# Performance work log

Hardware: AMD Instinct MI355X
Metric: run time of the kernel (lower is better)

## Reference

```python
import jax, jax.numpy as jnp
import numpy as np

FRAME_LEN = 400
HOP = 160
FFT_LEN = 512
PREEMPH = 0.97
MEL_FLOOR = 1.192092955078125e-07


def _hertz_to_mel(freq):
    return 1127.0 * np.log(1.0 + freq / 700.0)


def _mel_filter_bank(num_frequency_bins=256, num_mel_filters=80, min_frequency=20.0,
                     max_frequency=8000.0, sampling_rate=16000):
    mel_min = _hertz_to_mel(min_frequency)
    mel_max = _hertz_to_mel(max_frequency)
    mel_freqs = np.linspace(mel_min, mel_max, num_mel_filters + 2)
    # NOTE: source has filter_freqs = mel_freqs (mel-space, intentional replication of bug)
    filter_freqs = mel_freqs
    fft_bin_width = sampling_rate / (num_frequency_bins * 2)
    fft_freqs = _hertz_to_mel(fft_bin_width * np.arange(num_frequency_bins))
    filter_diff = np.diff(filter_freqs)
    slopes = filter_freqs[None, :] - fft_freqs[:, None]          # [256, 82]
    down_slopes = -slopes[:, :-2] / filter_diff[:-1]
    up_slopes = slopes[:, 2:] / filter_diff[1:]
    fb = np.maximum(0.0, np.minimum(down_slopes, up_slopes))      # [256, 80]
    # F.pad(mel_filters, (0,0,0,1)) -> one extra zero row -> [257, 80]
    return np.pad(fb, ((0, 1), (0, 0))).astype(np.float32)


def _window():
    n = np.arange(FRAME_LEN)
    hann = 0.5 - 0.5 * np.cos(2.0 * np.pi * n / (FRAME_LEN - 1))  # periodic=False
    return (hann ** 0.85).astype(np.float32)


def setup_inputs() -> dict:
    key = jax.random.key(0)
    T = 9_600_000  # 10 min @ 16 kHz
    raw_speech = jax.random.normal(key, (1, T), dtype=jnp.float32)
    return {
        "raw_speech": raw_speech,
        "mel_filters": jnp.asarray(_mel_filter_bank()),  # [257, 80]
        "window": jnp.asarray(_window()),                # [400]
    }


def reference(raw_speech, mel_filters, window):
    wav = raw_speech.reshape(-1) * 32768.0  # * 2**15
    num_frames = 1 + (wav.shape[0] - FRAME_LEN) // HOP
    idx = jnp.arange(num_frames)[:, None] * HOP + jnp.arange(FRAME_LEN)[None, :]
    frames = wav[idx]                                         # [F, 400]
    frames = frames - frames.mean(axis=1, keepdims=True)      # remove DC offset
    # preemphasis: y[0] = x[0]*(1-p), y[n] = x[n] - p*x[n-1]
    pre = jnp.concatenate(
        [frames[:, :1] * (1.0 - PREEMPH), frames[:, 1:] - PREEMPH * frames[:, :-1]],
        axis=1,
    )
    pre = pre * window
    padded = jnp.pad(pre, ((0, 0), (0, FFT_LEN - FRAME_LEN)))  # [F, 512]
    spec = jnp.abs(jnp.fft.rfft(padded, axis=1)) ** 2          # [F, 257]
    mel = jnp.log(jnp.maximum(spec @ mel_filters, MEL_FLOOR))  # [F, 80]
    mean = mel.mean(axis=0, keepdims=True)
    var = mel.var(axis=0, keepdims=True, ddof=1)               # unbiased
    return (mel - mean) / jnp.sqrt(var + 1e-7)
```

## Files before the change

### kernel.cpp

```cpp
#include <hip/hip_runtime.h>
#include <math.h>

#define FRAME_LEN 400
#define HOP 160
#define NMEL 80
#define PREEMPH 0.97f
#define MEL_FLOOR 1.192092955078125e-07f
#define WAVES 4
#define PPW 4
#define PPB (WAVES*PPW)

__device__ __forceinline__ float2 cadd(float2 a, float2 b){ return make_float2(a.x+b.x, a.y+b.y); }
__device__ __forceinline__ float2 csub(float2 a, float2 b){ return make_float2(a.x-b.x, a.y-b.y); }
__device__ __forceinline__ float2 cmul(float2 a, float2 b){ return make_float2(a.x*b.x-a.y*b.y, a.x*b.y+a.y*b.x); }

__device__ __forceinline__ float bperm(int addr, float v) {
    return __int_as_float(__builtin_amdgcn_ds_bpermute(addr, __float_as_int(v)));
}
template<int C>
__device__ __forceinline__ float dppf(float v) {
    return __int_as_float(__builtin_amdgcn_update_dpp(0, __float_as_int(v), C, 0xF, 0xF, false));
}
__device__ __forceinline__ float wscan_add(float v) {
    v += __int_as_float(__builtin_amdgcn_update_dpp(0, __float_as_int(v), 0x111, 0xF, 0xF, false));
    v += __int_as_float(__builtin_amdgcn_update_dpp(0, __float_as_int(v), 0x112, 0xF, 0xF, false));
    v += __int_as_float(__builtin_amdgcn_update_dpp(0, __float_as_int(v), 0x114, 0xF, 0xF, false));
    v += __int_as_float(__builtin_amdgcn_update_dpp(0, __float_as_int(v), 0x118, 0xF, 0xF, false));
    v += __int_as_float(__builtin_amdgcn_update_dpp(0, __float_as_int(v), 0x142, 0xA, 0xF, false));
    v += __int_as_float(__builtin_amdgcn_update_dpp(0, __float_as_int(v), 0x143, 0xC, 0xF, false));
    return v;
}

__global__ __launch_bounds__(256) void feat_kernel(
    const float* __restrict__ raw, const float* __restrict__ window,
    float* __restrict__ mel_out, double* __restrict__ accum, int F)
{
    __shared__ __align__(16) float wlds[FRAME_LEN];
    __shared__ __align__(16) float xu[WAVES][560];
    __shared__ __align__(16) float pfx[WAVES][2][256];

    float* uu = xu[0];
    int*   ks = (int*)xu[1];

    const int t = threadIdx.x;
    const int l = t & 63;
    const int w = t >> 6;

    if (t < FRAME_LEN) wlds[t] = window[t] * 32768.f;
    if (t + 256 < FRAME_LEN) wlds[t + 256] = window[t + 256] * 32768.f;
    const double mel_min = 1127.0 * log(1.0 + 20.0 / 700.0);
    const double mel_max = 1127.0 * log(1.0 + 8000.0 / 700.0);
    const double dstep = (mel_max - mel_min) / 81.0;
    {
        double fhz = 31.25 * (double)t;
        double m = 1127.0 * log(1.0 + fhz / 700.0);
        uu[t] = (float)((m - mel_min) / dstep);
    }
    __syncthreads();
    if (t < 82) {
        double fhz = 700.0 * (exp((mel_min + (double)t * dstep) / 1127.0) - 1.0);
        int k = (int)ceil(fhz / 31.25);
        k = max(0, min(256, k));
        while (k > 0 && uu[k - 1] >= (float)t) --k;
        while (k < 256 && uu[k] < (float)t) ++k;
        ks[t] = k;
    }

    const int bl   = __brev((unsigned)l) >> 26;
    const int adrX = (l ^ 63) << 2;
    const int adr0 = ((64 - l) & 63) << 2;

    float2 dt[5];
    float  sg[6];
    #pragma unroll
    for (int j = 0; j < 6; ++j) {
        int d = 1 << j;
        sg[j] = (l & d) ? -1.f : 1.f;
        if (j >= 1) {
            float2 tw = make_float2(1.f, 0.f);
            if (l & d) {
                float tt = (float)(l & (d - 1));
                float ang = -3.1415926535897932f * tt / (float)d;
                sincosf(ang, &tw.y, &tw.x);
            }
            dt[j - 1] = tw;
        }
    }
    float2 w2[4];
    #pragma unroll
    for (int q = 1; q < 4; ++q) {
        float ang = -6.283185307179586f * (float)(bl * q) * (1.0f / 256.0f);
        sincosf(ang, &w2[q].y, &w2[q].x);
    }
    float2 wk[4];
    #pragma unroll
    for (int q = 0; q < 4; ++q) {
        int k = 4 * l + q;
        float ang = -3.1415926535897932f * (float)k * (1.0f / 256.0f);
        sincosf(ang, &wk[q].y, &wk[q].x);
    }
    __syncthreads();

    float fr1[4];
    #pragma unroll
    for (int q = 0; q < 4; ++q) {
        float u = uu[4 * l + q];
        fr1[q] = u - floorf(u);
    }
    int a0 = ks[l], b0 = ks[l + 1], e0 = ks[l + 2];
    int a1 = 1, b1 = 1, e1 = 1;
    if (l < 16) { a1 = ks[64 + l]; b1 = ks[65 + l]; e1 = ks[66 + l]; }
    __syncthreads();

    float* xw = xu[w];
    const int NP = (F + 1) >> 1;
    const int basePair = blockIdx.x * PPB + w * PPW;

    float acc_s0 = 0.f, acc_q0 = 0.f;
    float acc_s1 = 0.f, acc_q1 = 0.f;

    for (int fi = 0; fi < PPW; ++fi) {
        int P = basePair + fi;
        if (P >= NP) break;
        int fA = 2 * P;
        bool hasB = (fA + 1) < F;

        const float4* g4 = (const float4*)(raw + (size_t)fA * HOP);
        float4 a = g4[l];
        float4 b = make_float4(0.f, 0.f, 0.f, 0.f);
        float4 c = make_float4(0.f, 0.f, 0.f, 0.f);
        if (hasB || l < 36) b = g4[64 + l];
        if (hasB && l < 12) c = g4[128 + l];
        float as = a.x + a.y + a.z + a.w;
        float bs = b.x + b.y + b.z + b.w;
        float cs = c.x + c.y + c.z + c.w;
        float sA8 = as + (l < 36 ? bs : 0.f);
        float sB8 = (l >= 40 ? as : 0.f) + bs + cs;
        float totA = __int_as_float(__builtin_amdgcn_readlane(__float_as_int(wscan_add(sA8)), 63));
        float totB = __int_as_float(__builtin_amdgcn_readlane(__float_as_int(wscan_add(sB8)), 63));
        float KA = totA * (1.0f / (float)FRAME_LEN) * (1.0f - PREEMPH);
        float KB = totB * (1.0f / (float)FRAME_LEN) * (1.0f - PREEMPH);

        ((float4*)xw)[l] = a;
        ((float4*)xw)[64 + l] = b;
        if (l < 12) ((float4*)xw)[128 + l] = c;

        float2 Z[2][4];
        #pragma unroll
        for (int r = 0; r < 4; ++r) {
            int off = 128 * r + 2 * bl;
            if (off < FRAME_LEN) {
                float2 xA = *(const float2*)(xw + off);
                float2 xB = *(const float2*)(xw + 160 + off);
                float xm1A = (off == 0) ? xA.x : xw[off - 1];
                float xm1B = (off == 0) ? xB.x : xw[159 + off];
                float2 wn  = *(const float2*)(wlds + off);
                Z[0][r] = make_float2((fmaf(-PREEMPH, xm1A, xA.x) - KA) * wn.x,
                                      (fmaf(-PREEMPH, xA.x,  xA.y) - KA) * wn.y);
                Z[1][r] = make_float2((fmaf(-PREEMPH, xm1B, xB.x) - KB) * wn.x,
                                      (fmaf(-PREEMPH, xB.x,  xB.y) - KB) * wn.y);
            } else {
                Z[0][r] = make_float2(0.f, 0.f);
                Z[1][r] = make_float2(0.f, 0.f);
            }
        }

        #pragma unroll
        for (int s = 0; s < 2; ++s) {
            float2 t0 = cadd(Z[s][0], Z[s][2]);
            float2 t1 = csub(Z[s][0], Z[s][2]);
            float2 t2 = cadd(Z[s][1], Z[s][3]);
            float2 t3 = csub(Z[s][1], Z[s][3]);
            Z[s][0] = cadd(t0, t2);
            Z[s][2] = csub(t0, t2);
            Z[s][1] = make_float2(t1.x + t3.y, t1.y - t3.x);
            Z[s][3] = make_float2(t1.x - t3.y, t1.y + t3.x);
            #pragma unroll
            for (int q = 1; q < 4; ++q) Z[s][q] = cmul(Z[s][q], w2[q]);
        }

        #pragma unroll
        for (int s = 0; s < 2; ++s)
        #pragma unroll
        for (int q = 0; q < 4; ++q) {
            float ox = dppf<0xB1>(Z[s][q].x), oy = dppf<0xB1>(Z[s][q].y);
            Z[s][q].x = fmaf(sg[0], Z[s][q].x, ox);
            Z[s][q].y = fmaf(sg[0], Z[s][q].y, oy);
        }
        #pragma unroll
        for (int s = 0; s < 2; ++s)
        #pragma unroll
        for (int q = 0; q < 4; ++q) {
            float2 Zw = cmul(Z[s][q], dt[0]);
            float ox = dppf<0x4E>(Zw.x), oy = dppf<0x4E>(Zw.y);
            Z[s][q].x = fmaf(sg[1], Zw.x, ox);
            Z[s][q].y = fmaf(sg[1], Zw.y, oy);
        }
        #pragma unroll
        for (int s = 0; s < 2; ++s)
        #pragma unroll
        for (int q = 0; q < 4; ++q) {
            float2 Zw = cmul(Z[s][q], dt[1]);
            float ox = __shfl_xor(Zw.x, 4, 64), oy = __shfl_xor(Zw.y, 4, 64);
            Z[s][q].x = fmaf(sg[2], Zw.x, ox);
            Z[s][q].y = fmaf(sg[2], Zw.y, oy);
        }
        #pragma unroll
        for (int s = 0; s < 2; ++s)
        #pragma unroll
        for (int q = 0; q < 4; ++q) {
            float2 Zw = cmul(Z[s][q], dt[2]);
            float ox = dppf<0x128>(Zw.x), oy = dppf<0x128>(Zw.y);
            Z[s][q].x = fmaf(sg[3], Zw.x, ox);
            Z[s][q].y = fmaf(sg[3], Zw.y, oy);
        }
        #pragma unroll
        for (int s = 0; s < 2; ++s)
        #pragma unroll
        for (int q = 0; q < 4; ++q) {
            float2 Zw = cmul(Z[s][q], dt[3]);
            float ox = __shfl_xor(Zw.x, 16, 64), oy = __shfl_xor(Zw.y, 16, 64);
            Z[s][q].x = fmaf(sg[4], Zw.x, ox);
            Z[s][q].y = fmaf(sg[4], Zw.y, oy);
        }
        #pragma unroll
        for (int s = 0; s < 2; ++s)
        #pragma unroll
        for (int q = 0; q < 4; ++q) {
            float2 Zw = cmul(Z[s][q], dt[4]);
            float ox = __shfl_xor(Zw.x, 32, 64), oy = __shfl_xor(Zw.y, 32, 64);
            Z[s][q].x = fmaf(sg[5], Zw.x, ox);
            Z[s][q].y = fmaf(sg[5], Zw.y, oy);
        }

        #pragma unroll
        for (int s = 0; s < 2; ++s) {
            float zcr[4], zci[4];
            zcr[0] = bperm(adr0, Z[s][0].x);
            zci[0] = bperm(adr0, Z[s][0].y);
            zcr[1] = bperm(adrX, Z[s][3].x);
            zci[1] = bperm(adrX, Z[s][3].y);
            zcr[2] = bperm(adrX, Z[s][2].x);
            zci[2] = bperm(adrX, Z[s][2].y);
            zcr[3] = bperm(adrX, Z[s][1].x);
            zci[3] = bperm(adrX, Z[s][1].y);

            float pw[4], pv[4];
            #pragma unroll
            for (int q = 0; q < 4; ++q) {
                float Er = 0.5f * (Z[s][q].x + zcr[q]);
                float Ei = 0.5f * (Z[s][q].y - zci[q]);
                float Or = 0.5f * (Z[s][q].y + zci[q]);
                float Oi = 0.5f * (zcr[q] - Z[s][q].x);
                float Xr = Er + Or * wk[q].x - Oi * wk[q].y;
                float Xi = Ei + Or * wk[q].y + Oi * wk[q].x;
                pw[q] = Xr * Xr + Xi * Xi;
                pv[q] = pw[q] * fr1[q];
            }
            float A0 = pw[0], A1 = A0 + pw[1], A2 = A1 + pw[2], A3 = A2 + pw[3];
            float B0 = pv[0], B1 = B0 + pv[1], B2 = B1 + pv[2], B3 = B2 + pv[3];
            float sA = wscan_add(A3);
            float sB = wscan_add(B3);
            float exA = sA - A3;
            float exB = sB - B3;
            float* pP = pfx[w][0];
            float* pF = pfx[w][1];
            ((float4*)pP)[l] = make_float4(exA + A0, exA + A1, exA + A2, exA + A3);
            ((float4*)pF)[l] = make_float4(exB + B0, exB + B1, exB + B2, exB + B3);

            int f = fA + s;
            bool act = (s == 0) || hasB;
            if (act) {
                float E1a = pF[a0 - 1], E1b = pF[b0 - 1], E1e = pF[e0 - 1];
                float EAb = pP[b0 - 1], EAe = pP[e0 - 1];
                float acc = fmaf(2.f, E1b, -E1a) - E1e + (EAe - EAb);
                float v = __logf(fmaxf(acc, MEL_FLOOR));
                mel_out[(size_t)f * NMEL + l] = v;
                acc_s0 += v; acc_q0 = fmaf(v, v, acc_q0);
                if (l < 16) {
                    float F1a = pF[a1 - 1], F1b = pF[b1 - 1], F1e = pF[e1 - 1];
                    float FAb = pP[b1 - 1], FAe = pP[e1 - 1];
                    float ac2 = fmaf(2.f, F1b, -F1a) - F1e + (FAe - FAb);
                    float v1 = __logf(fmaxf(ac2, MEL_FLOOR));
                    mel_out[(size_t)f * NMEL + 64 + l] = v1;
                    acc_s1 += v1; acc_q1 = fmaf(v1, v1, acc_q1);
                }
            }
        }
    }

    {
        float* red = pfx[w][0];
        red[l] = acc_s0;
        red[80 + l] = acc_q0;
        if (l < 16) { red[64 + l] = acc_s1; red[144 + l] = acc_q1; }
    }
    __syncthreads();
    if (t < 160) {
        float tot = pfx[0][0][t] + pfx[1][0][t] + pfx[2][0][t] + pfx[3][0][t];
        atomicAdd(&accum[t], (double)tot);
    }
}

__global__ __launch_bounds__(256) void norm_kernel(
    float* __restrict__ mel, const double* __restrict__ accum, int F)
{
    __shared__ float s_mean[NMEL], s_inv[NMEL];
    int t = threadIdx.x;
    if (t < NMEL) {
        double S = accum[t], Q = accum[NMEL + t];
        double mean = S / (double)F;
        double var = (Q - S * S / (double)F) / (double)(F - 1);
        s_mean[t] = (float)mean;
        s_inv[t]  = (float)(1.0 / sqrt(var + 1e-7));
    }
    __syncthreads();
    unsigned n = (unsigned)F * NMEL;
    unsigned stride = gridDim.x * 256u * 4u;
    unsigned i = (blockIdx.x * 256u + (unsigned)t) * 4u;
    int c = (int)(i % NMEL);
    float m0 = s_mean[c],     r0 = s_inv[c];
    float m1 = s_mean[c + 1], r1 = s_inv[c + 1];
    float m2 = s_mean[c + 2], r2 = s_inv[c + 2];
    float m3 = s_mean[c + 3], r3 = s_inv[c + 3];
    for (; i < n; i += stride) {
        float4 v = *(float4*)(mel + i);
        v.x = (v.x - m0) * r0;
        v.y = (v.y - m1) * r1;
        v.z = (v.z - m2) * r2;
        v.w = (v.w - m3) * r3;
        *(float4*)(mel + i) = v;
    }
}

extern "C" void kernel_launch(void* const* d_in, const int* in_sizes, int n_in,
                              void* d_out, int out_size, void* d_ws, size_t ws_size,
                              hipStream_t stream)
{
    const float* raw = (const float*)d_in[0];
    const float* window = (const float*)d_in[2];
    float* out = (float*)d_out;

    int N = in_sizes[0];
    int F = 1 + (N - FRAME_LEN) / HOP;
    double* accum = (double*)d_ws;

    hipMemsetAsync(d_ws, 0, 2 * NMEL * sizeof(double), stream);
    int NP = (F + 1) / 2;
    int gridA = (NP + PPB - 1) / PPB;
    feat_kernel<<<gridA, 256, 0, stream>>>(raw, window, out, accum, F);
    norm_kernel<<<2560, 256, 0, stream>>>(out, accum, F);
}
```

Baseline: 153.8 us.

## Process four overlapping frames per wave iteration instead of two

Each wave now loads a 880-sample window covering four consecutive frames (hop 160) and runs the FFT, power and mel stages on four frames at once, where it previously handled two. This raises reuse of the loaded samples, since four frames need 880 samples instead of 2x560, and gives more independent work per iteration to hide latency. In exchange, register pressure roughly doubles (Z[4][4] complex values), and LDS grows, with prefix buffers double-buffered by frame parity. The tail uses bounds-checked loads against N/4.

```diff
diff --git a/kernel.cpp b/kernel.cpp
--- a/kernel.cpp
+++ b/kernel.cpp
@@ -7,8 +7,8 @@
 #define PREEMPH 0.97f
 #define MEL_FLOOR 1.192092955078125e-07f
 #define WAVES 4
-#define PPW 4
-#define PPB (WAVES*PPW)
+#define QPW 2
+#define QPB (WAVES*QPW)
 
 __device__ __forceinline__ float2 cadd(float2 a, float2 b){ return make_float2(a.x+b.x, a.y+b.y); }
 __device__ __forceinline__ float2 csub(float2 a, float2 b){ return make_float2(a.x-b.x, a.y-b.y); }
@@ -33,11 +33,11 @@
 
 __global__ __launch_bounds__(256) void feat_kernel(
     const float* __restrict__ raw, const float* __restrict__ window,
-    float* __restrict__ mel_out, double* __restrict__ accum, int F)
+    float* __restrict__ mel_out, double* __restrict__ accum, int F, int N4)
 {
     __shared__ __align__(16) float wlds[FRAME_LEN];
-    __shared__ __align__(16) float xu[WAVES][560];
-    __shared__ __align__(16) float pfx[WAVES][2][256];
+    __shared__ __align__(16) float xu[WAVES][880];
+    __shared__ __align__(16) float pfx[WAVES][2][2][256];
 
     float* uu = xu[0];
     int*   ks = (int*)xu[1];
@@ -113,60 +113,75 @@
     __syncthreads();
 
     float* xw = xu[w];
-    const int NP = (F + 1) >> 1;
-    const int basePair = blockIdx.x * PPB + w * PPW;
+    const int NQ = (F + 3) >> 2;
+    const int baseQ = blockIdx.x * QPB + w * QPW;
 
     float acc_s0 = 0.f, acc_q0 = 0.f;
     float acc_s1 = 0.f, acc_q1 = 0.f;
 
-    for (int fi = 0; fi < PPW; ++fi) {
-        int P = basePair + fi;
-        if (P >= NP) break;
-        int fA = 2 * P;
-        bool hasB = (fA + 1) < F;
-
-        const float4* g4 = (const float4*)(raw + (size_t)fA * HOP);
-        float4 a = g4[l];
-        float4 b = make_float4(0.f, 0.f, 0.f, 0.f);
-        float4 c = make_float4(0.f, 0.f, 0.f, 0.f);
-        if (hasB || l < 36) b = g4[64 + l];
-        if (hasB && l < 12) c = g4[128 + l];
+    for (int fi = 0; fi < QPW; ++fi) {
+        int Q = baseQ + fi;
+        if (Q >= NQ) break;
+        int f0 = 4 * Q;
+        int nf = min(4, F - f0);
+
+        const float4* g4 = (const float4*)(raw + (size_t)f0 * HOP);
+        float4 a, b, c, d;
+        if (nf == 4) {
+            a = g4[l];
+            b = g4[64 + l];
+            c = g4[128 + l];
+            d = make_float4(0.f, 0.f, 0.f, 0.f);
+            if (l < 28) d = g4[192 + l];
+        } else {
+            int base4 = Q * 160;
+            a = b = c = d = make_float4(0.f, 0.f, 0.f, 0.f);
+            if (base4 + l < N4)        a = g4[l];
+            if (base4 + 64 + l < N4)   b = g4[64 + l];
+            if (base4 + 128 + l < N4)  c = g4[128 + l];
+            if (l < 28 && base4 + 192 + l < N4) d = g4[192 + l];
+        }
         float as = a.x + a.y + a.z + a.w;
         float bs = b.x + b.y + b.z + b.w;
         float cs = c.x + c.y + c.z + c.w;
-        float sA8 = as + (l < 36 ? bs : 0.f);
-        float sB8 = (l >= 40 ? as : 0.f) + bs + cs;
-        float totA = __int_as_float(__builtin_amdgcn_readlane(__float_as_int(wscan_add(sA8)), 63));
-        float totB = __int_as_float(__builtin_amdgcn_readlane(__float_as_int(wscan_add(sB8)), 63));
-        float KA = totA * (1.0f / (float)FRAME_LEN) * (1.0f - PREEMPH);
-        float KB = totB * (1.0f / (float)FRAME_LEN) * (1.0f - PREEMPH);
+        float ds = d.x + d.y + d.z + d.w;
+        float p0 = as + (l < 36 ? bs : 0.f);
+        float p1 = (l >= 40 ? as : 0.f) + bs + (l < 12 ? cs : 0.f);
+        float p2 = (l >= 16 ? bs : 0.f) + (l < 52 ? cs : 0.f);
+        float p3 = (l >= 56 ? bs : 0.f) + cs + (l < 28 ? ds : 0.f);
+        const float KC = (1.0f / (float)FRAME_LEN) * (1.0f - PREEMPH);
+        float K[4];
+        K[0] = __int_as_float(__builtin_amdgcn_readlane(__float_as_int(wscan_add(p0)), 63)) * KC;
+        K[1] = __int_as_float(__builtin_amdgcn_readlane(__float_as_int(wscan_add(p1)), 63)) * KC;
+        K[2] = __int_as_float(__builtin_amdgcn_readlane(__float_as_int(wscan_add(p2)), 63)) * KC;
+        K[3] = __int_as_float(__builtin_amdgcn_readlane(__float_as_int(wscan_add(p3)), 63)) * KC;
 
         ((float4*)xw)[l] = a;
         ((float4*)xw)[64 + l] = b;
-        if (l < 12) ((float4*)xw)[128 + l] = c;
-
-        float2 Z[2][4];
+        ((float4*)xw)[128 + l] = c;
+        if (l < 28) ((float4*)xw)[192 + l] = d;
+
+        float2 Z[4][4];
         #pragma unroll
         for (int r = 0; r < 4; ++r) {
             int off = 128 * r + 2 * bl;
             if (off < FRAME_LEN) {
-                float2 xA = *(const float2*)(xw + off);
-                float2 xB = *(const float2*)(xw + 160 + off);
-                float xm1A = (off == 0) ? xA.x : xw[off - 1];
-                float xm1B = (off == 0) ? xB.x : xw[159 + off];
-                float2 wn  = *(const float2*)(wlds + off);
-                Z[0][r] = make_float2((fmaf(-PREEMPH, xm1A, xA.x) - KA) * wn.x,
-                                      (fmaf(-PREEMPH, xA.x,  xA.y) - KA) * wn.y);
-                Z[1][r] = make_float2((fmaf(-PREEMPH, xm1B, xB.x) - KB) * wn.x,
-                                      (fmaf(-PREEMPH, xB.x,  xB.y) - KB) * wn.y);
+                float2 wn = *(const float2*)(wlds + off);
+                #pragma unroll
+                for (int s = 0; s < 4; ++s) {
+                    float2 x = *(const float2*)(xw + 160 * s + off);
+                    float xm1 = (off == 0) ? x.x : xw[160 * s + off - 1];
+                    Z[s][r] = make_float2((fmaf(-PREEMPH, xm1, x.x) - K[s]) * wn.x,
+                                          (fmaf(-PREEMPH, x.x,  x.y) - K[s]) * wn.y);
+                }
             } else {
-                Z[0][r] = make_float2(0.f, 0.f);
-                Z[1][r] = make_float2(0.f, 0.f);
+                #pragma unroll
+                for (int s = 0; s < 4; ++s) Z[s][r] = make_float2(0.f, 0.f);
             }
         }
 
         #pragma unroll
-        for (int s = 0; s < 2; ++s) {
+        for (int s = 0; s < 4; ++s) {
             float2 t0 = cadd(Z[s][0], Z[s][2]);
             float2 t1 = csub(Z[s][0], Z[s][2]);
             float2 t2 = cadd(Z[s][1], Z[s][3]);
@@ -180,7 +195,7 @@
         }
 
         #pragma unroll
-        for (int s = 0; s < 2; ++s)
+        for (int s = 0; s < 4; ++s)
         #pragma unroll
         for (int q = 0; q < 4; ++q) {
             float ox = dppf<0xB1>(Z[s][q].x), oy = dppf<0xB1>(Z[s][q].y);
@@ -188,7 +203,7 @@
             Z[s][q].y = fmaf(sg[0], Z[s][q].y, oy);
         }
         #pragma unroll
-        for (int s = 0; s < 2; ++s)
+        for (int s = 0; s < 4; ++s)
         #pragma unroll
         for (int q = 0; q < 4; ++q) {
             float2 Zw = cmul(Z[s][q], dt[0]);
@@ -197,7 +212,7 @@
             Z[s][q].y = fmaf(sg[1], Zw.y, oy);
         }
         #pragma unroll
-        for (int s = 0; s < 2; ++s)
+        for (int s = 0; s < 4; ++s)
         #pragma unroll
         for (int q = 0; q < 4; ++q) {
             float2 Zw = cmul(Z[s][q], dt[1]);
@@ -206,7 +221,7 @@
             Z[s][q].y = fmaf(sg[2], Zw.y, oy);
         }
         #pragma unroll
-        for (int s = 0; s < 2; ++s)
+        for (int s = 0; s < 4; ++s)
         #pragma unroll
         for (int q = 0; q < 4; ++q) {
             float2 Zw = cmul(Z[s][q], dt[2]);
@@ -215,7 +230,7 @@
             Z[s][q].y = fmaf(sg[3], Zw.y, oy);
         }
         #pragma unroll
-        for (int s = 0; s < 2; ++s)
+        for (int s = 0; s < 4; ++s)
         #pragma unroll
         for (int q = 0; q < 4; ++q) {
             float2 Zw = cmul(Z[s][q], dt[3]);
@@ -224,7 +239,7 @@
             Z[s][q].y = fmaf(sg[4], Zw.y, oy);
         }
         #pragma unroll
-        for (int s = 0; s < 2; ++s)
+        for (int s = 0; s < 4; ++s)
         #pragma unroll
         for (int q = 0; q < 4; ++q) {
             float2 Zw = cmul(Z[s][q], dt[4]);
@@ -234,7 +249,7 @@
         }
 
         #pragma unroll
-        for (int s = 0; s < 2; ++s) {
+        for (int s = 0; s < 4; ++s) {
             float zcr[4], zci[4];
             zcr[0] = bperm(adr0, Z[s][0].x);
             zci[0] = bperm(adr0, Z[s][0].y);
@@ -263,14 +278,13 @@
             float sB = wscan_add(B3);
             float exA = sA - A3;
             float exB = sB - B3;
-            float* pP = pfx[w][0];
-            float* pF = pfx[w][1];
+            float* pP = pfx[w][s & 1][0];
+            float* pF = pfx[w][s & 1][1];
             ((float4*)pP)[l] = make_float4(exA + A0, exA + A1, exA + A2, exA + A3);
             ((float4*)pF)[l] = make_float4(exB + B0, exB + B1, exB + B2, exB + B3);
 
-            int f = fA + s;
-            bool act = (s == 0) || hasB;
-            if (act) {
+            if (s < nf) {
+                int f = f0 + s;
                 float E1a = pF[a0 - 1], E1b = pF[b0 - 1], E1e = pF[e0 - 1];
                 float EAb = pP[b0 - 1], EAe = pP[e0 - 1];
                 float acc = fmaf(2.f, E1b, -E1a) - E1e + (EAe - EAb);
@@ -290,14 +304,14 @@
     }
 
     {
-        float* red = pfx[w][0];
+        float* red = pfx[w][0][0];
         red[l] = acc_s0;
         red[80 + l] = acc_q0;
         if (l < 16) { red[64 + l] = acc_s1; red[144 + l] = acc_q1; }
     }
     __syncthreads();
     if (t < 160) {
-        float tot = pfx[0][0][t] + pfx[1][0][t] + pfx[2][0][t] + pfx[3][0][t];
+        float tot = pfx[0][0][0][t] + pfx[1][0][0][t] + pfx[2][0][0][t] + pfx[3][0][0][t];
         atomicAdd(&accum[t], (double)tot);
     }
 }
@@ -346,8 +360,8 @@
     double* accum = (double*)d_ws;
 
     hipMemsetAsync(d_ws, 0, 2 * NMEL * sizeof(double), stream);
-    int NP = (F + 1) / 2;
-    int gridA = (NP + PPB - 1) / PPB;
-    feat_kernel<<<gridA, 256, 0, stream>>>(raw, window, out, accum, F);
+    int NQ = (F + 3) / 4;
+    int gridA = (NQ + QPB - 1) / QPB;
+    feat_kernel<<<gridA, 256, 0, stream>>>(raw, window, out, accum, F, N / 4);
     norm_kernel<<<2560, 256, 0, stream>>>(out, accum, F);
 }
```

After: 167.1 us. +8.6%, slower.

## Use single-wave blocks, precompute mel tables once, and shard stats atomics

Applied to the files above, without the earlier changes.

Moves the per-block double-precision mel bin table setup into a separate one-block setup kernel whose outputs go to workspace. The feature kernel becomes 64-thread single-wave blocks with no __syncthreads and 4x as many blocks. Each wave atomically adds its statistics straight into one of 8 shadow accumulators, and the norm kernel sums them. This removes redundant per-block transcendental setup and block barriers, at the cost of 4x more double atomics and an extra kernel launch.

```diff
diff --git a/kernel.cpp b/kernel.cpp
--- a/kernel.cpp
+++ b/kernel.cpp
@@ -6,9 +6,8 @@
 #define NMEL 80
 #define PREEMPH 0.97f
 #define MEL_FLOOR 1.192092955078125e-07f
-#define WAVES 4
 #define PPW 4
-#define PPB (WAVES*PPW)
+#define NSHADOW 8
 
 __device__ __forceinline__ float2 cadd(float2 a, float2 b){ return make_float2(a.x+b.x, a.y+b.y); }
 __device__ __forceinline__ float2 csub(float2 a, float2 b){ return make_float2(a.x-b.x, a.y-b.y); }
@@ -31,23 +30,11 @@
     return v;
 }
 
-__global__ __launch_bounds__(256) void feat_kernel(
-    const float* __restrict__ raw, const float* __restrict__ window,
-    float* __restrict__ mel_out, double* __restrict__ accum, int F)
+__global__ __launch_bounds__(256) void setup_kernel(float* __restrict__ frtab,
+                                                    int* __restrict__ kstab)
 {
-    __shared__ __align__(16) float wlds[FRAME_LEN];
-    __shared__ __align__(16) float xu[WAVES][560];
-    __shared__ __align__(16) float pfx[WAVES][2][256];
-
-    float* uu = xu[0];
-    int*   ks = (int*)xu[1];
-
-    const int t = threadIdx.x;
-    const int l = t & 63;
-    const int w = t >> 6;
-
-    if (t < FRAME_LEN) wlds[t] = window[t] * 32768.f;
-    if (t + 256 < FRAME_LEN) wlds[t + 256] = window[t + 256] * 32768.f;
+    __shared__ float uu[256];
+    int t = threadIdx.x;
     const double mel_min = 1127.0 * log(1.0 + 20.0 / 700.0);
     const double mel_max = 1127.0 * log(1.0 + 8000.0 / 700.0);
     const double dstep = (mel_max - mel_min) / 81.0;
@@ -57,14 +44,32 @@
         uu[t] = (float)((m - mel_min) / dstep);
     }
     __syncthreads();
+    {
+        float u = uu[t];
+        frtab[t] = u - floorf(u);
+    }
     if (t < 82) {
         double fhz = 700.0 * (exp((mel_min + (double)t * dstep) / 1127.0) - 1.0);
         int k = (int)ceil(fhz / 31.25);
         k = max(0, min(256, k));
         while (k > 0 && uu[k - 1] >= (float)t) --k;
         while (k < 256 && uu[k] < (float)t) ++k;
-        ks[t] = k;
-    }
+        kstab[t] = k;
+    }
+}
+
+__global__ __launch_bounds__(64) void feat_kernel(
+    const float* __restrict__ raw, const float* __restrict__ window,
+    float* __restrict__ mel_out, double* __restrict__ accum,
+    const float* __restrict__ frtab, const int* __restrict__ kstab, int F)
+{
+    __shared__ __align__(16) float wlds[FRAME_LEN];
+    __shared__ __align__(16) float xu[560];
+    __shared__ __align__(16) float pfx[2][256];
+
+    const int l = threadIdx.x;
+
+    for (int i = l; i < FRAME_LEN; i += 64) wlds[i] = window[i] * 32768.f;
 
     const int bl   = __brev((unsigned)l) >> 26;
     const int adrX = (l ^ 63) << 2;
@@ -99,22 +104,18 @@
         float ang = -3.1415926535897932f * (float)k * (1.0f / 256.0f);
         sincosf(ang, &wk[q].y, &wk[q].x);
     }
-    __syncthreads();
 
     float fr1[4];
-    #pragma unroll
-    for (int q = 0; q < 4; ++q) {
-        float u = uu[4 * l + q];
-        fr1[q] = u - floorf(u);
-    }
-    int a0 = ks[l], b0 = ks[l + 1], e0 = ks[l + 2];
+    {
+        float4 fv = *(const float4*)(frtab + 4 * l);
+        fr1[0] = fv.x; fr1[1] = fv.y; fr1[2] = fv.z; fr1[3] = fv.w;
+    }
+    int a0 = kstab[l], b0 = kstab[l + 1], e0 = kstab[l + 2];
     int a1 = 1, b1 = 1, e1 = 1;
-    if (l < 16) { a1 = ks[64 + l]; b1 = ks[65 + l]; e1 = ks[66 + l]; }
-    __syncthreads();
-
-    float* xw = xu[w];
+    if (l < 16) { a1 = kstab[64 + l]; b1 = kstab[65 + l]; e1 = kstab[66 + l]; }
+
     const int NP = (F + 1) >> 1;
-    const int basePair = blockIdx.x * PPB + w * PPW;
+    const int basePair = blockIdx.x * PPW;
 
     float acc_s0 = 0.f, acc_q0 = 0.f;
     float acc_s1 = 0.f, acc_q1 = 0.f;
@@ -141,19 +142,19 @@
         float KA = totA * (1.0f / (float)FRAME_LEN) * (1.0f - PREEMPH);
         float KB = totB * (1.0f / (float)FRAME_LEN) * (1.0f - PREEMPH);
 
-        ((float4*)xw)[l] = a;
-        ((float4*)xw)[64 + l] = b;
-        if (l < 12) ((float4*)xw)[128 + l] = c;
+        ((float4*)xu)[l] = a;
+        ((float4*)xu)[64 + l] = b;
+        if (l < 12) ((float4*)xu)[128 + l] = c;
 
         float2 Z[2][4];
         #pragma unroll
         for (int r = 0; r < 4; ++r) {
             int off = 128 * r + 2 * bl;
             if (off < FRAME_LEN) {
-                float2 xA = *(const float2*)(xw + off);
-                float2 xB = *(const float2*)(xw + 160 + off);
-                float xm1A = (off == 0) ? xA.x : xw[off - 1];
-                float xm1B = (off == 0) ? xB.x : xw[159 + off];
+                float2 xA = *(const float2*)(xu + off);
+                float2 xB = *(const float2*)(xu + 160 + off);
+                float xm1A = (off == 0) ? xA.x : xu[off - 1];
+                float xm1B = (off == 0) ? xB.x : xu[159 + off];
                 float2 wn  = *(const float2*)(wlds + off);
                 Z[0][r] = make_float2((fmaf(-PREEMPH, xm1A, xA.x) - KA) * wn.x,
                                       (fmaf(-PREEMPH, xA.x,  xA.y) - KA) * wn.y);
@@ -263,8 +264,8 @@
             float sB = wscan_add(B3);
             float exA = sA - A3;
             float exB = sB - B3;
-            float* pP = pfx[w][0];
-            float* pF = pfx[w][1];
+            float* pP = pfx[0];
+            float* pF = pfx[1];
             ((float4*)pP)[l] = make_float4(exA + A0, exA + A1, exA + A2, exA + A3);
             ((float4*)pF)[l] = make_float4(exB + B0, exB + B1, exB + B2, exB + B3);
 
@@ -289,16 +290,12 @@
         }
     }
 
-    {
-        float* red = pfx[w][0];
-        red[l] = acc_s0;
-        red[80 + l] = acc_q0;
-        if (l < 16) { red[64 + l] = acc_s1; red[144 + l] = acc_q1; }
-    }
-    __syncthreads();
-    if (t < 160) {
-        float tot = pfx[0][0][t] + pfx[1][0][t] + pfx[2][0][t] + pfx[3][0][t];
-        atomicAdd(&accum[t], (double)tot);
+    double* A = accum + (blockIdx.x & (NSHADOW - 1)) * 160;
+    atomicAdd(&A[l], (double)acc_s0);
+    atomicAdd(&A[80 + l], (double)acc_q0);
+    if (l < 16) {
+        atomicAdd(&A[64 + l], (double)acc_s1);
+        atomicAdd(&A[144 + l], (double)acc_q1);
     }
 }
 
@@ -308,7 +305,12 @@
     __shared__ float s_mean[NMEL], s_inv[NMEL];
     int t = threadIdx.x;
     if (t < NMEL) {
-        double S = accum[t], Q = accum[NMEL + t];
+        double S = 0.0, Q = 0.0;
+        #pragma unroll
+        for (int j = 0; j < NSHADOW; ++j) {
+            S += accum[j * 160 + t];
+            Q += accum[j * 160 + 80 + t];
+        }
         double mean = S / (double)F;
         double var = (Q - S * S / (double)F) / (double)(F - 1);
         s_mean[t] = (float)mean;
@@ -343,11 +345,15 @@
 
     int N = in_sizes[0];
     int F = 1 + (N - FRAME_LEN) / HOP;
+
     double* accum = (double*)d_ws;
-
-    hipMemsetAsync(d_ws, 0, 2 * NMEL * sizeof(double), stream);
+    float*  frtab = (float*)((char*)d_ws + NSHADOW * 160 * sizeof(double));
+    int*    kstab = (int*)((char*)d_ws + NSHADOW * 160 * sizeof(double) + 256 * sizeof(float));
+
+    hipMemsetAsync(d_ws, 0, NSHADOW * 160 * sizeof(double), stream);
+    setup_kernel<<<1, 256, 0, stream>>>(frtab, kstab);
     int NP = (F + 1) / 2;
-    int gridA = (NP + PPB - 1) / PPB;
-    feat_kernel<<<gridA, 256, 0, stream>>>(raw, window, out, accum, F);
+    int gridA = (NP + PPW - 1) / PPW;
+    feat_kernel<<<gridA, 64, 0, stream>>>(raw, window, out, accum, frtab, kstab, F);
     norm_kernel<<<2560, 256, 0, stream>>>(out, accum, F);
 }
```

New measurement: 150.0 us. 2.5% less time.
